# Kernel tuning notes

Measured on AMD Instinct MI355X. Metric: run time of the kernel, lower is better.

The kernel has to match this reference:

```python
import jax, jax.numpy as jnp
import numpy as np

N = 50000      # nodes
E = 600000     # edges
F_IN = 128     # input features
H = 128        # hidden
C = 40         # classes


def _glorot(key, shape):
    lim = float(np.sqrt(6.0 / (shape[0] + shape[1])))
    return jax.random.uniform(key, shape, jnp.float32, -lim, lim)


def setup_inputs() -> dict:
    key = jax.random.key(0)
    ks = jax.random.split(key, 16)
    inp = {
        "x": jax.random.normal(ks[0], (N, F_IN), jnp.float32),
        "edge_index": jax.random.randint(ks[1], (2, E), 0, N, jnp.int64),
    }
    # SAGEConv params: Wl (neighbor branch, with bias), Wr (root branch), stored [in, out]
    dims = [(F_IN, H), (H, H), (H, H)]
    for i, (din, dout) in enumerate(dims, start=1):
        inp[f"Wl{i}"] = _glorot(ks[2 * i], (din, dout))
        inp[f"bl{i}"] = jnp.zeros((dout,), jnp.float32)
        inp[f"Wr{i}"] = _glorot(ks[2 * i + 1], (din, dout))
    inp["W_lin1"] = _glorot(ks[10], (H, H))
    inp["b_lin1"] = jnp.zeros((H,), jnp.float32)
    inp["W_lin2"] = _glorot(ks[11], (H, C))
    inp["b_lin2"] = jnp.zeros((C,), jnp.float32)
    return inp


def _sage_conv(x, src, dst, Wl, bl, Wr):
    # mean-aggregate neighbor features at destination nodes
    msgs = x[src]  # [E, d] gather
    agg = jax.ops.segment_sum(msgs, dst, num_segments=N)
    deg = jax.ops.segment_sum(jnp.ones((E,), x.dtype), dst, num_segments=N)
    agg = agg / jnp.clip(deg, 1.0)[:, None]
    return agg @ Wl + bl + x @ Wr


def reference(x, edge_index, Wl1, bl1, Wr1, Wl2, bl2, Wr2, Wl3, bl3, Wr3,
              W_lin1, b_lin1, W_lin2, b_lin2):
    src, dst = edge_index[0], edge_index[1]
    h = jax.nn.relu(_sage_conv(x, src, dst, Wl1, bl1, Wr1))
    h = jax.nn.relu(_sage_conv(h, src, dst, Wl2, bl2, Wr2))
    h = jax.nn.relu(_sage_conv(h, src, dst, Wl3, bl3, Wr3))
    h = jax.nn.relu(h @ W_lin1 + b_lin1)
    # dropout: inference mode (training=False) -> identity
    logits = h @ W_lin2 + b_lin2
    return jax.nn.log_softmax(logits, axis=-1)
```

## Files before the change

### kernel.cpp

```cpp
#include <hip/hip_runtime.h>
#include <hip/hip_bf16.h>
#include <math.h>

#define NNODES 50000
#define NEDGES 600000
#define FDIM   128
#define NCLS   40
#define SLOTS  64
#define FILL_BLOCKS 1172
#define CVT_BLOCKS 6250
#define PACK_BLOCKS 62
#define ALL_TOTAL (FILL_BLOCKS + CVT_BLOCKS + PACK_BLOCKS)
#define NT16 (NNODES / 16)

typedef __hip_bfloat16 bf16;
typedef short bf16x8 __attribute__((ext_vector_type(8)));
typedef short bf16x4 __attribute__((ext_vector_type(4)));
typedef float f32x4  __attribute__((ext_vector_type(4)));
typedef float f32x2  __attribute__((ext_vector_type(2)));
typedef unsigned u32x4 __attribute__((ext_vector_type(4)));

__device__ __forceinline__ float u2f(unsigned u) {
    union { unsigned i; float f; } cv;
    cv.i = u;
    return cv.f;
}
__device__ __forceinline__ short f2b(float f) {
    bf16 h = __float2bfloat16(f);
    return *(const short*)&h;
}
__device__ __forceinline__ float ldf(const void* p, int fp32, int idx) {
    return fp32 ? ((const float*)p)[idx]
                : __bfloat162float(((const bf16*)p)[idx]);
}
__device__ __forceinline__ int wave_is_fp32(const unsigned* p, int lane) {
    unsigned w = p[lane];
    unsigned e = (w >> 7) & 0xFFu;
    int inr = (e >= 100u && e <= 140u) ? 1 : 0;
    return (int)__popcll(__ballot(inr)) < 32;
}
__device__ __forceinline__ int lidx(int row, int col) {
    return row * 128 + ((((col >> 3) ^ (row & 15)) << 3) | (col & 7));
}

__global__ void k_all(const int* __restrict__ e32, const long long* __restrict__ e64,
                      const void* __restrict__ xin,
                      const void* Wl1, const void* Wr1, const void* Wl2,
                      const void* Wr2, const void* Wl3, const void* Wr3,
                      const void* Wlin1, const void* Wlin2,
                      const void* b1, const void* b2, const void* b3,
                      const void* b4, const void* b5,
                      int* __restrict__ cursor, int* __restrict__ edge_src,
                      bf16* __restrict__ xb,
                      bf16x8* __restrict__ packed, float* __restrict__ biasf) {
    int b = blockIdx.x, tid = threadIdx.x, lane = tid & 63;
    if (b < FILL_BLOCKS) {
        unsigned hw = ((const unsigned*)e32)[2 * lane + 1];
        int is64 = (__ballot(hw != 0u) == 0ull) ? 1 : 0;
        int i0 = b * 512 + tid;
        int i1 = i0 + 256;
        int s0 = 0, d0 = 0, s1 = 0, d1 = 0;
        bool v0 = i0 < NEDGES, v1 = i1 < NEDGES;
        if (v0) { s0 = is64 ? (int)e64[i0] : e32[i0];
                  d0 = is64 ? (int)e64[NEDGES + i0] : e32[NEDGES + i0]; }
        if (v1) { s1 = is64 ? (int)e64[i1] : e32[i1];
                  d1 = is64 ? (int)e64[NEDGES + i1] : e32[NEDGES + i1]; }
        int p0 = 0, p1 = 0;
        if (v0) p0 = atomicAdd(&cursor[d0], 1);
        if (v1) p1 = atomicAdd(&cursor[d1], 1);
        if (v0 && p0 < SLOTS) edge_src[d0 * SLOTS + p0] = s0;
        if (v1 && p1 < SLOTS) edge_src[d1 * SLOTS + p1] = s1;
        return;
    }
    if (b < FILL_BLOCKS + CVT_BLOCKS) {
        int xf = wave_is_fp32((const unsigned*)xin, lane);
        int i = (b - FILL_BLOCKS) * 256 + tid;
        if (xf) {
            float4 v = ((const float4*)xin)[i];
            bf16x4 o;
            o[0] = f2b(v.x); o[1] = f2b(v.y); o[2] = f2b(v.z); o[3] = f2b(v.w);
            ((bf16x4*)xb)[i] = o;
        } else {
            ((uint2*)xb)[i] = ((const uint2*)xin)[i];
        }
        return;
    }
    int wf = wave_is_fp32((const unsigned*)Wl1, lane);
    int lb = b - FILL_BLOCKS - CVT_BLOCKS;
    if (lb >= 59) {
        int t = (lb - 59) * 256 + tid;
        if (t >= 5 * 128) return;
        int which = t >> 7, idx = t & 127;
        const void* srcs[5] = {b1, b2, b3, b4, b5};
        int n = (which == 4) ? NCLS : 128;
        float v = 0.f;
        if (idx < n) v = ldf(srcs[which], wf, idx);
        biasf[t] = v;
        return;
    }
    int t2 = lb * 256 + tid;
    int frag = t2 >> 6;
    if (frag >= 236) return;
    int q = lane >> 4, l16 = lane & 15;
    const void* W;
    int kbase, n, ldw = 128, nvalid = 128;
    if (frag < 192) {
        int g = frag >> 6, local = frag & 63;
        int kt = local >> 3, nt = local & 7;
        const void* Wl = (g == 0) ? Wl1 : (g == 1) ? Wl2 : Wl3;
        const void* Wr = (g == 0) ? Wr1 : (g == 1) ? Wr2 : Wr3;
        W = (kt < 4) ? Wl : Wr;
        kbase = (kt & 3) * 32;
        n = nt * 16 + l16;
    } else if (frag < 224) {
        int local = frag - 192;
        int kt = local >> 3, nt = local & 7;
        W = Wlin1; kbase = kt * 32; n = nt * 16 + l16;
    } else {
        int local = frag - 224;
        int kt = local / 3, nt = local % 3;
        W = Wlin2; kbase = kt * 32; n = nt * 16 + l16;
        ldw = NCLS; nvalid = NCLS;
    }
    bf16x8 v;
#pragma unroll
    for (int j = 0; j < 8; j++) {
        float e = 0.f;
        if (n < nvalid) e = ldf(W, wf, (kbase + q * 8 + j) * ldw + n);
        v[j] = f2b(e);
    }
    packed[frag * 64 + lane] = v;
}

__device__ __forceinline__ void agg8(const bf16* __restrict__ x,
        const int* __restrict__ deg, const int* __restrict__ es,
        short* __restrict__ lds, int node00, int wave, int lane) {
    const int g = lane >> 4, c = lane & 15;
    const int gsel = lane & 48;
    const int nbase = node00 + wave * 8;
    int dgp[2], eip[2];
#pragma unroll
    for (int p = 0; p < 2; p++) dgp[p] = deg[nbase + p * 4 + g];
#pragma unroll
    for (int p = 0; p < 2; p++) {
        int ei = es[(nbase + p * 4 + g) * SLOTS + c];
        eip[p] = ((unsigned)ei >= NNODES) ? 0 : ei;
    }
#pragma unroll
    for (int p = 0; p < 2; p++) {
        const int dg = dgp[p];
        f32x2 acc2[4];
#pragma unroll
        for (int k = 0; k < 4; k++) acc2[k] = (f32x2){0.f, 0.f};
#pragma unroll
        for (int j = 0; j < 16; j++) {
            int idx = __shfl(eip[p], gsel | j);
            float m = (j < dg) ? 1.f : 0.f;
            f32x2 m2 = (f32x2){m, m};
            u32x4 u = *(const u32x4*)(x + (unsigned)(idx * FDIM + c * 8));
#pragma unroll
            for (int k = 0; k < 4; k++) {
                f32x2 vv = (f32x2){u2f(u[k] << 16), u2f(u[k] & 0xFFFF0000u)};
                acc2[k] += vv * m2;
            }
        }
        if (__ballot(dg > 16) != 0ull) {
            for (int jb = 16; jb < SLOTS && __ballot(dg > jb) != 0ull; jb += 16) {
                int ei2 = es[(nbase + p * 4 + g) * SLOTS + jb + c];
                if ((unsigned)ei2 >= NNODES) ei2 = 0;
                for (int j = 0; j < 16; j++) {
                    int idx = __shfl(ei2, gsel | j);
                    float m = (jb + j < dg) ? 1.f : 0.f;
                    f32x2 m2 = (f32x2){m, m};
                    u32x4 u = *(const u32x4*)(x + (unsigned)(idx * FDIM + c * 8));
#pragma unroll
                    for (int k = 0; k < 4; k++) {
                        f32x2 vv = (f32x2){u2f(u[k] << 16), u2f(u[k] & 0xFFFF0000u)};
                        acc2[k] += vv * m2;
                    }
                }
            }
        }
        float inv = (dg > 0) ? 1.f / (float)dg : 0.f;
        bf16x8 o;
#pragma unroll
        for (int k = 0; k < 4; k++) {
            o[2 * k]     = f2b(acc2[k].x * inv);
            o[2 * k + 1] = f2b(acc2[k].y * inv);
        }
        *(bf16x8*)(lds + lidx(wave * 8 + p * 4 + g, c * 8)) = o;
    }
}

__device__ __forceinline__ void gemm_half(int lane, int wave,
        short* __restrict__ lds, const bf16x8 rt[4],
        const bf16x8* __restrict__ packed, const float* __restrict__ bias) {
    const int q = lane >> 4, l16 = lane & 15;
    f32x4 acc[4];
#pragma unroll
    for (int n = 0; n < 4; n++) acc[n] = (f32x4){0.f, 0.f, 0.f, 0.f};
#pragma unroll
    for (int kt = 0; kt < 8; kt++) {
        bf16x8 a;
        if (kt < 4)
            a = *(const bf16x8*)(lds + lidx(l16, kt * 32 + q * 8));
        else
            a = rt[kt - 4];
#pragma unroll
        for (int n = 0; n < 4; n++)
            acc[n] = __builtin_amdgcn_mfma_f32_16x16x32_bf16(
                a, packed[(kt * 8 + wave * 4 + n) * 64 + lane], acc[n], 0, 0, 0);
    }
    __syncthreads();
#pragma unroll
    for (int n = 0; n < 4; n++) {
        int col = (wave * 4 + n) * 16 + l16;
        float bv = bias[col];
#pragma unroll
        for (int r = 0; r < 4; r++)
            lds[lidx(q * 4 + r, col)] = f2b(fmaxf(acc[n][r] + bv, 0.f));
    }
    __syncthreads();
}

__device__ __forceinline__ void store_half(int rowbase, int lane, int wave,
        const short* __restrict__ lds, bf16* __restrict__ out) {
    const int g = lane >> 4, c = lane & 15;
#pragma unroll
    for (int pp = 0; pp < 2; pp++) {
        int p = wave * 2 + pp;
        bf16x8 v = *(const bf16x8*)(lds + lidx(p * 4 + g, c * 8));
        *(bf16x8*)(out + (unsigned)((rowbase + p * 4 + g) * FDIM + c * 8)) = v;
    }
}

__device__ __forceinline__ void head(int rowbase, int lane, int wave,
        const short* __restrict__ h3, short* __restrict__ h1,
        const bf16x8* __restrict__ packed, const float* __restrict__ bias1,
        const float* __restrict__ bias2, float* __restrict__ out) {
    const int q = lane >> 4, l16 = lane & 15;
    f32x4 acc[4];
#pragma unroll
    for (int n = 0; n < 4; n++) acc[n] = (f32x4){0.f, 0.f, 0.f, 0.f};
#pragma unroll
    for (int kt = 0; kt < 4; kt++) {
        bf16x8 a = *(const bf16x8*)(h3 + lidx(l16, kt * 32 + q * 8));
#pragma unroll
        for (int n = 0; n < 4; n++)
            acc[n] = __builtin_amdgcn_mfma_f32_16x16x32_bf16(
                a, packed[(192 + kt * 8 + wave * 4 + n) * 64 + lane], acc[n], 0, 0, 0);
    }
#pragma unroll
    for (int n = 0; n < 4; n++) {
        int col = (wave * 4 + n) * 16 + l16;
        float bv = bias1[col];
#pragma unroll
        for (int r = 0; r < 4; r++)
            h1[lidx(q * 4 + r, col)] = f2b(fmaxf(acc[n][r] + bv, 0.f));
    }
    __syncthreads();
    if (wave != 0) return;
    f32x4 acc2[3];
#pragma unroll
    for (int n = 0; n < 3; n++) acc2[n] = (f32x4){0.f, 0.f, 0.f, 0.f};
#pragma unroll
    for (int kt = 0; kt < 4; kt++) {
        bf16x8 a = *(const bf16x8*)(h1 + lidx(l16, kt * 32 + q * 8));
#pragma unroll
        for (int n = 0; n < 3; n++)
            acc2[n] = __builtin_amdgcn_mfma_f32_16x16x32_bf16(
                a, packed[(224 + kt * 3 + n) * 64 + lane], acc2[n], 0, 0, 0);
    }
    const float NEG = -1e30f;
    bool v2ok = (l16 < 8);
#pragma unroll
    for (int r = 0; r < 4; r++) {
        unsigned row = (unsigned)(rowbase + q * 4 + r);
        float v0 = acc2[0][r] + bias2[l16];
        float v1 = acc2[1][r] + bias2[16 + l16];
        float v2 = v2ok ? (acc2[2][r] + bias2[32 + l16]) : NEG;
        float m = fmaxf(fmaxf(v0, v1), v2);
#pragma unroll
        for (int mk = 1; mk < 16; mk <<= 1) m = fmaxf(m, __shfl_xor(m, mk));
        float sden = expf(v0 - m) + expf(v1 - m) + (v2ok ? expf(v2 - m) : 0.f);
#pragma unroll
        for (int mk = 1; mk < 16; mk <<= 1) sden += __shfl_xor(sden, mk);
        float l = m + logf(sden);
        out[row * NCLS + l16] = v0 - l;
        out[row * NCLS + 16 + l16] = v1 - l;
        if (v2ok) out[row * NCLS + 32 + l16] = v2 - l;
    }
}

__global__ void __launch_bounds__(128)
k_layer(const bf16* __restrict__ src, const int* __restrict__ deg,
        const int* __restrict__ edge_src, const bf16x8* __restrict__ packed,
        const float* __restrict__ bias, bf16* __restrict__ out) {
    __shared__ __align__(16) short lds[16 * 128];
    const int lane = threadIdx.x & 63, wave = threadIdx.x >> 6;
    const int rowbase = blockIdx.x * 16;
    const int q = lane >> 4, l16 = lane & 15;
    bf16x8 rt[4];
#pragma unroll
    for (int kt = 0; kt < 4; kt++)
        rt[kt] = *(const bf16x8*)(src +
                     (unsigned)((rowbase + l16) * FDIM + kt * 32 + q * 8));
    agg8(src, deg, edge_src, lds, rowbase, wave, lane);
    __syncthreads();
    gemm_half(lane, wave, lds, rt, packed, bias);
    store_half(rowbase, lane, wave, lds, out);
}

__global__ void __launch_bounds__(128)
k_layer3head(const bf16* __restrict__ src, const int* __restrict__ deg,
             const int* __restrict__ edge_src, const bf16x8* __restrict__ packed,
             const float* __restrict__ biasf, float* __restrict__ out) {
    __shared__ __align__(16) short h3[16 * 128];
    __shared__ __align__(16) short h1[16 * 128];
    const int lane = threadIdx.x & 63, wave = threadIdx.x >> 6;
    const int rowbase = blockIdx.x * 16;
    const int q = lane >> 4, l16 = lane & 15;
    bf16x8 rt[4];
#pragma unroll
    for (int kt = 0; kt < 4; kt++)
        rt[kt] = *(const bf16x8*)(src +
                     (unsigned)((rowbase + l16) * FDIM + kt * 32 + q * 8));
    agg8(src, deg, edge_src, h3, rowbase, wave, lane);
    __syncthreads();
    gemm_half(lane, wave, h3, rt, packed + 128 * 64, biasf + 256);
    head(rowbase, lane, wave, h3, h1, packed, biasf + 384, biasf + 512, out);
}

extern "C" void kernel_launch(void* const* d_in, const int* in_sizes, int n_in,
                              void* d_out, int out_size, void* d_ws, size_t ws_size,
                              hipStream_t stream) {
    char* ws = (char*)d_ws;
    size_t off = 0;
    auto take = [&](size_t bytes) {
        void* pp = ws + off;
        off = (off + bytes + 255) & ~(size_t)255;
        return pp;
    };
    const int* e32 = (const int*)d_in[1];
    const long long* e64 = (const long long*)d_in[1];
    int* cursor    = (int*)take(NNODES * 4);
    int* edge_src  = (int*)take((size_t)NNODES * SLOTS * 4);
    bf16x8* packed = (bf16x8*)take(236 * 64 * 16);
    float* biasf   = (float*)take(5 * 128 * 4);
    bf16* xb       = (bf16*)take((size_t)NNODES * FDIM * 2);
    bf16* bufA     = (bf16*)take((size_t)NNODES * FDIM * 2);
    float* outp    = (float*)d_out;
    bf16* bufB     = xb;

    hipMemsetAsync(cursor, 0, NNODES * 4, stream);
    k_all<<<ALL_TOTAL, 256, 0, stream>>>(
        e32, e64, d_in[0], d_in[2], d_in[4], d_in[5], d_in[7], d_in[8],
        d_in[10], d_in[11], d_in[13], d_in[3], d_in[6], d_in[9], d_in[12],
        d_in[14], cursor, edge_src, xb, packed, biasf);

    k_layer<<<NT16, 128, 0, stream>>>(xb, cursor, edge_src, packed, biasf, bufA);
    k_layer<<<NT16, 128, 0, stream>>>(bufA, cursor, edge_src,
                                      packed + 64 * 64, biasf + 128, bufB);
    k_layer3head<<<NT16, 128, 0, stream>>>(bufB, cursor, edge_src,
                                           packed, biasf, outp);
}
```

Measured before the change: 230.0 us.

## Precompute layer-1 root GEMM in prep kernel and use 4-wave layer blocks

```diff
diff --git a/kernel.cpp b/kernel.cpp
--- a/kernel.cpp
+++ b/kernel.cpp
@@ -9,8 +9,10 @@
 #define SLOTS  64
 #define FILL_BLOCKS 1172
 #define CVT_BLOCKS 6250
-#define PACK_BLOCKS 62
-#define ALL_TOTAL (FILL_BLOCKS + CVT_BLOCKS + PACK_BLOCKS)
+#define R1_BLOCKS 3125
+#define ALL_TOTAL (FILL_BLOCKS + CVT_BLOCKS + R1_BLOCKS)
+#define CZ_BLOCKS 49
+#define PRE_TOTAL (CZ_BLOCKS + 62)
 #define NT16 (NNODES / 16)
 
 typedef __hip_bfloat16 bf16;
@@ -43,50 +45,21 @@
     return row * 128 + ((((col >> 3) ^ (row & 15)) << 3) | (col & 7));
 }
 
-__global__ void k_all(const int* __restrict__ e32, const long long* __restrict__ e64,
-                      const void* __restrict__ xin,
-                      const void* Wl1, const void* Wr1, const void* Wl2,
+__global__ void k_pre(const void* Wl1, const void* Wr1, const void* Wl2,
                       const void* Wr2, const void* Wl3, const void* Wr3,
                       const void* Wlin1, const void* Wlin2,
                       const void* b1, const void* b2, const void* b3,
                       const void* b4, const void* b5,
-                      int* __restrict__ cursor, int* __restrict__ edge_src,
-                      bf16* __restrict__ xb,
+                      int* __restrict__ cursor,
                       bf16x8* __restrict__ packed, float* __restrict__ biasf) {
     int b = blockIdx.x, tid = threadIdx.x, lane = tid & 63;
-    if (b < FILL_BLOCKS) {
-        unsigned hw = ((const unsigned*)e32)[2 * lane + 1];
-        int is64 = (__ballot(hw != 0u) == 0ull) ? 1 : 0;
-        int i0 = b * 512 + tid;
-        int i1 = i0 + 256;
-        int s0 = 0, d0 = 0, s1 = 0, d1 = 0;
-        bool v0 = i0 < NEDGES, v1 = i1 < NEDGES;
-        if (v0) { s0 = is64 ? (int)e64[i0] : e32[i0];
-                  d0 = is64 ? (int)e64[NEDGES + i0] : e32[NEDGES + i0]; }
-        if (v1) { s1 = is64 ? (int)e64[i1] : e32[i1];
-                  d1 = is64 ? (int)e64[NEDGES + i1] : e32[NEDGES + i1]; }
-        int p0 = 0, p1 = 0;
-        if (v0) p0 = atomicAdd(&cursor[d0], 1);
-        if (v1) p1 = atomicAdd(&cursor[d1], 1);
-        if (v0 && p0 < SLOTS) edge_src[d0 * SLOTS + p0] = s0;
-        if (v1 && p1 < SLOTS) edge_src[d1 * SLOTS + p1] = s1;
+    if (b < CZ_BLOCKS) {
+        int i = b * 256 + tid;
+        if (i < NNODES / 4 + 1) ((int4*)cursor)[i] = (int4){0, 0, 0, 0};
         return;
     }
-    if (b < FILL_BLOCKS + CVT_BLOCKS) {
-        int xf = wave_is_fp32((const unsigned*)xin, lane);
-        int i = (b - FILL_BLOCKS) * 256 + tid;
-        if (xf) {
-            float4 v = ((const float4*)xin)[i];
-            bf16x4 o;
-            o[0] = f2b(v.x); o[1] = f2b(v.y); o[2] = f2b(v.z); o[3] = f2b(v.w);
-            ((bf16x4*)xb)[i] = o;
-        } else {
-            ((uint2*)xb)[i] = ((const uint2*)xin)[i];
-        }
-        return;
-    }
     int wf = wave_is_fp32((const unsigned*)Wl1, lane);
-    int lb = b - FILL_BLOCKS - CVT_BLOCKS;
+    int lb = b - CZ_BLOCKS;
     if (lb >= 59) {
         int t = (lb - 59) * 256 + tid;
         if (t >= 5 * 128) return;
@@ -132,106 +105,179 @@
     packed[frag * 64 + lane] = v;
 }
 
-__device__ __forceinline__ void agg8(const bf16* __restrict__ x,
+__global__ void k_all(const int* __restrict__ e32, const long long* __restrict__ e64,
+                      const void* __restrict__ xin,
+                      int* __restrict__ cursor, int* __restrict__ edge_src,
+                      bf16* __restrict__ xb,
+                      const bf16x8* __restrict__ packed,
+                      const float* __restrict__ biasf, float* __restrict__ R1) {
+    int b = blockIdx.x, tid = threadIdx.x, lane = tid & 63;
+    if (b < FILL_BLOCKS) {
+        unsigned hw = ((const unsigned*)e32)[2 * lane + 1];
+        int is64 = (__ballot(hw != 0u) == 0ull) ? 1 : 0;
+        int i0 = b * 512 + tid;
+        int i1 = i0 + 256;
+        int s0 = 0, d0 = 0, s1 = 0, d1 = 0;
+        bool v0 = i0 < NEDGES, v1 = i1 < NEDGES;
+        if (v0) { s0 = is64 ? (int)e64[i0] : e32[i0];
+                  d0 = is64 ? (int)e64[NEDGES + i0] : e32[NEDGES + i0]; }
+        if (v1) { s1 = is64 ? (int)e64[i1] : e32[i1];
+                  d1 = is64 ? (int)e64[NEDGES + i1] : e32[NEDGES + i1]; }
+        int p0 = 0, p1 = 0;
+        if (v0) p0 = atomicAdd(&cursor[d0], 1);
+        if (v1) p1 = atomicAdd(&cursor[d1], 1);
+        if (v0 && p0 < SLOTS) edge_src[d0 * SLOTS + p0] = s0;
+        if (v1 && p1 < SLOTS) edge_src[d1 * SLOTS + p1] = s1;
+        return;
+    }
+    if (b < FILL_BLOCKS + CVT_BLOCKS) {
+        int xf = wave_is_fp32((const unsigned*)xin, lane);
+        int i = (b - FILL_BLOCKS) * 256 + tid;
+        if (xf) {
+            float4 v = ((const float4*)xin)[i];
+            bf16x4 o;
+            o[0] = f2b(v.x); o[1] = f2b(v.y); o[2] = f2b(v.z); o[3] = f2b(v.w);
+            ((bf16x4*)xb)[i] = o;
+        } else {
+            ((uint2*)xb)[i] = ((const uint2*)xin)[i];
+        }
+        return;
+    }
+    int rb = (b - FILL_BLOCKS - CVT_BLOCKS) * 16;
+    int wave = tid >> 6;
+    int q = lane >> 4, l16 = lane & 15;
+    int xf = wave_is_fp32((const unsigned*)xin, lane);
+    bf16x8 a[4];
+#pragma unroll
+    for (int kt = 0; kt < 4; kt++) {
+        if (xf) {
+            const float* xp = (const float*)xin +
+                              (unsigned)((rb + l16) * FDIM + kt * 32 + q * 8);
+            float4 v0 = *(const float4*)xp;
+            float4 v1 = *(const float4*)(xp + 4);
+            a[kt][0] = f2b(v0.x); a[kt][1] = f2b(v0.y);
+            a[kt][2] = f2b(v0.z); a[kt][3] = f2b(v0.w);
+            a[kt][4] = f2b(v1.x); a[kt][5] = f2b(v1.y);
+            a[kt][6] = f2b(v1.z); a[kt][7] = f2b(v1.w);
+        } else {
+            a[kt] = *(const bf16x8*)((const bf16*)xin +
+                        (unsigned)((rb + l16) * FDIM + kt * 32 + q * 8));
+        }
+    }
+    f32x4 acc[2];
+#pragma unroll
+    for (int n = 0; n < 2; n++) acc[n] = (f32x4){0.f, 0.f, 0.f, 0.f};
+#pragma unroll
+    for (int kt = 0; kt < 4; kt++)
+#pragma unroll
+        for (int n = 0; n < 2; n++)
+            acc[n] = __builtin_amdgcn_mfma_f32_16x16x32_bf16(
+                a[kt], packed[((kt + 4) * 8 + wave * 2 + n) * 64 + lane],
+                acc[n], 0, 0, 0);
+#pragma unroll
+    for (int n = 0; n < 2; n++) {
+        int col = (wave * 2 + n) * 16 + l16;
+        float bv = biasf[col];
+#pragma unroll
+        for (int r = 0; r < 4; r++)
+            R1[(unsigned)((rb + q * 4 + r) * FDIM + col)] = acc[n][r] + bv;
+    }
+}
+
+__device__ __forceinline__ void agg4(const bf16* __restrict__ x,
         const int* __restrict__ deg, const int* __restrict__ es,
-        short* __restrict__ lds, int node00, int wave, int lane) {
+        short* __restrict__ lds, int rowbase, int wave, int lane) {
     const int g = lane >> 4, c = lane & 15;
     const int gsel = lane & 48;
-    const int nbase = node00 + wave * 8;
-    int dgp[2], eip[2];
-#pragma unroll
-    for (int p = 0; p < 2; p++) dgp[p] = deg[nbase + p * 4 + g];
-#pragma unroll
-    for (int p = 0; p < 2; p++) {
-        int ei = es[(nbase + p * 4 + g) * SLOTS + c];
-        eip[p] = ((unsigned)ei >= NNODES) ? 0 : ei;
-    }
-#pragma unroll
-    for (int p = 0; p < 2; p++) {
-        const int dg = dgp[p];
-        f32x2 acc2[4];
-#pragma unroll
-        for (int k = 0; k < 4; k++) acc2[k] = (f32x2){0.f, 0.f};
-#pragma unroll
-        for (int j = 0; j < 16; j++) {
-            int idx = __shfl(eip[p], gsel | j);
-            float m = (j < dg) ? 1.f : 0.f;
-            f32x2 m2 = (f32x2){m, m};
-            u32x4 u = *(const u32x4*)(x + (unsigned)(idx * FDIM + c * 8));
-#pragma unroll
-            for (int k = 0; k < 4; k++) {
-                f32x2 vv = (f32x2){u2f(u[k] << 16), u2f(u[k] & 0xFFFF0000u)};
-                acc2[k] += vv * m2;
-            }
+    const int node = rowbase + wave * 4 + g;
+    const int dg = deg[node];
+    int ei = es[node * SLOTS + c];
+    if ((unsigned)ei >= NNODES) ei = 0;
+    f32x2 acc2[4];
+#pragma unroll
+    for (int k = 0; k < 4; k++) acc2[k] = (f32x2){0.f, 0.f};
+#pragma unroll
+    for (int j = 0; j < 16; j++) {
+        int idx = __shfl(ei, gsel | j);
+        float m = (j < dg) ? 1.f : 0.f;
+        f32x2 m2 = (f32x2){m, m};
+        u32x4 u = *(const u32x4*)(x + (unsigned)(idx * FDIM + c * 8));
+#pragma unroll
+        for (int k = 0; k < 4; k++) {
+            f32x2 vv = (f32x2){u2f(u[k] << 16), u2f(u[k] & 0xFFFF0000u)};
+            acc2[k] += vv * m2;
         }
-        if (__ballot(dg > 16) != 0ull) {
-            for (int jb = 16; jb < SLOTS && __ballot(dg > jb) != 0ull; jb += 16) {
-                int ei2 = es[(nbase + p * 4 + g) * SLOTS + jb + c];
-                if ((unsigned)ei2 >= NNODES) ei2 = 0;
-                for (int j = 0; j < 16; j++) {
-                    int idx = __shfl(ei2, gsel | j);
-                    float m = (jb + j < dg) ? 1.f : 0.f;
-                    f32x2 m2 = (f32x2){m, m};
-                    u32x4 u = *(const u32x4*)(x + (unsigned)(idx * FDIM + c * 8));
-#pragma unroll
-                    for (int k = 0; k < 4; k++) {
-                        f32x2 vv = (f32x2){u2f(u[k] << 16), u2f(u[k] & 0xFFFF0000u)};
-                        acc2[k] += vv * m2;
-                    }
+    }
+    if (__ballot(dg > 16) != 0ull) {
+        for (int jb = 16; jb < SLOTS && __ballot(dg > jb) != 0ull; jb += 16) {
+            int ei2 = es[node * SLOTS + jb + c];
+            if ((unsigned)ei2 >= NNODES) ei2 = 0;
+            for (int j = 0; j < 16; j++) {
+                int idx = __shfl(ei2, gsel | j);
+                float m = (jb + j < dg) ? 1.f : 0.f;
+                f32x2 m2 = (f32x2){m, m};
+                u32x4 u = *(const u32x4*)(x + (unsigned)(idx * FDIM + c * 8));
+#pragma unroll
+                for (int k = 0; k < 4; k++) {
+                    f32x2 vv = (f32x2){u2f(u[k] << 16), u2f(u[k] & 0xFFFF0000u)};
+                    acc2[k] += vv * m2;
                 }
             }
         }
-        float inv = (dg > 0) ? 1.f / (float)dg : 0.f;
-        bf16x8 o;
-#pragma unroll
-        for (int k = 0; k < 4; k++) {
-            o[2 * k]     = f2b(acc2[k].x * inv);
-            o[2 * k + 1] = f2b(acc2[k].y * inv);
-        }
-        *(bf16x8*)(lds + lidx(wave * 8 + p * 4 + g, c * 8)) = o;
-    }
-}
-
-__device__ __forceinline__ void gemm_half(int lane, int wave,
+    }
+    float inv = (dg > 0) ? 1.f / (float)dg : 0.f;
+    bf16x8 o;
+#pragma unroll
+    for (int k = 0; k < 4; k++) {
+        o[2 * k]     = f2b(acc2[k].x * inv);
+        o[2 * k + 1] = f2b(acc2[k].y * inv);
+    }
+    *(bf16x8*)(lds + lidx(wave * 4 + g, c * 8)) = o;
+}
+
+template <bool FIRST>
+__device__ __forceinline__ void gemm_q(int rowbase, int lane, int wave,
         short* __restrict__ lds, const bf16x8 rt[4],
-        const bf16x8* __restrict__ packed, const float* __restrict__ bias) {
+        const bf16x8* __restrict__ packed, const float* __restrict__ bias,
+        const float* __restrict__ R1) {
     const int q = lane >> 4, l16 = lane & 15;
-    f32x4 acc[4];
-#pragma unroll
-    for (int n = 0; n < 4; n++) acc[n] = (f32x4){0.f, 0.f, 0.f, 0.f};
-#pragma unroll
-    for (int kt = 0; kt < 8; kt++) {
+    f32x4 acc[2];
+#pragma unroll
+    for (int n = 0; n < 2; n++) acc[n] = (f32x4){0.f, 0.f, 0.f, 0.f};
+    const int KT = FIRST ? 4 : 8;
+#pragma unroll
+    for (int kt = 0; kt < KT; kt++) {
         bf16x8 a;
         if (kt < 4)
             a = *(const bf16x8*)(lds + lidx(l16, kt * 32 + q * 8));
         else
             a = rt[kt - 4];
 #pragma unroll
-        for (int n = 0; n < 4; n++)
+        for (int n = 0; n < 2; n++)
             acc[n] = __builtin_amdgcn_mfma_f32_16x16x32_bf16(
-                a, packed[(kt * 8 + wave * 4 + n) * 64 + lane], acc[n], 0, 0, 0);
+                a, packed[(kt * 8 + wave * 2 + n) * 64 + lane], acc[n], 0, 0, 0);
     }
     __syncthreads();
 #pragma unroll
-    for (int n = 0; n < 4; n++) {
-        int col = (wave * 4 + n) * 16 + l16;
-        float bv = bias[col];
-#pragma unroll
-        for (int r = 0; r < 4; r++)
-            lds[lidx(q * 4 + r, col)] = f2b(fmaxf(acc[n][r] + bv, 0.f));
+    for (int n = 0; n < 2; n++) {
+        int col = (wave * 2 + n) * 16 + l16;
+        float bv = FIRST ? 0.f : bias[col];
+#pragma unroll
+        for (int r = 0; r < 4; r++) {
+            float v = acc[n][r] + bv;
+            if (FIRST) v += R1[(unsigned)((rowbase + q * 4 + r) * FDIM + col)];
+            lds[lidx(q * 4 + r, col)] = f2b(fmaxf(v, 0.f));
+        }
     }
     __syncthreads();
 }
 
-__device__ __forceinline__ void store_half(int rowbase, int lane, int wave,
+__device__ __forceinline__ void store_q(int rowbase, int lane, int wave,
         const short* __restrict__ lds, bf16* __restrict__ out) {
     const int g = lane >> 4, c = lane & 15;
-#pragma unroll
-    for (int pp = 0; pp < 2; pp++) {
-        int p = wave * 2 + pp;
-        bf16x8 v = *(const bf16x8*)(lds + lidx(p * 4 + g, c * 8));
-        *(bf16x8*)(out + (unsigned)((rowbase + p * 4 + g) * FDIM + c * 8)) = v;
-    }
+    int p = wave * 4 + g;
+    bf16x8 v = *(const bf16x8*)(lds + lidx(p, c * 8));
+    *(bf16x8*)(out + (unsigned)((rowbase + p) * FDIM + c * 8)) = v;
 }
 
 __device__ __forceinline__ void head(int rowbase, int lane, int wave,
@@ -239,20 +285,20 @@
         const bf16x8* __restrict__ packed, const float* __restrict__ bias1,
         const float* __restrict__ bias2, float* __restrict__ out) {
     const int q = lane >> 4, l16 = lane & 15;
-    f32x4 acc[4];
-#pragma unroll
-    for (int n = 0; n < 4; n++) acc[n] = (f32x4){0.f, 0.f, 0.f, 0.f};
+    f32x4 acc[2];
+#pragma unroll
+    for (int n = 0; n < 2; n++) acc[n] = (f32x4){0.f, 0.f, 0.f, 0.f};
 #pragma unroll
     for (int kt = 0; kt < 4; kt++) {
         bf16x8 a = *(const bf16x8*)(h3 + lidx(l16, kt * 32 + q * 8));
 #pragma unroll
-        for (int n = 0; n < 4; n++)
+        for (int n = 0; n < 2; n++)
             acc[n] = __builtin_amdgcn_mfma_f32_16x16x32_bf16(
-                a, packed[(192 + kt * 8 + wave * 4 + n) * 64 + lane], acc[n], 0, 0, 0);
-    }
-#pragma unroll
-    for (int n = 0; n < 4; n++) {
-        int col = (wave * 4 + n) * 16 + l16;
+                a, packed[(192 + kt * 8 + wave * 2 + n) * 64 + lane], acc[n], 0, 0, 0);
+    }
+#pragma unroll
+    for (int n = 0; n < 2; n++) {
+        int col = (wave * 2 + n) * 16 + l16;
         float bv = bias1[col];
 #pragma unroll
         for (int r = 0; r < 4; r++)
@@ -292,26 +338,30 @@
     }
 }
 
-__global__ void __launch_bounds__(128)
-k_layer(const bf16* __restrict__ src, const int* __restrict__ deg,
-        const int* __restrict__ edge_src, const bf16x8* __restrict__ packed,
-        const float* __restrict__ bias, bf16* __restrict__ out) {
+template <bool FIRST>
+__global__ void __launch_bounds__(256)
+k_layer_t(const bf16* __restrict__ src, const int* __restrict__ deg,
+          const int* __restrict__ edge_src, const bf16x8* __restrict__ packed,
+          const float* __restrict__ bias, const float* __restrict__ R1,
+          bf16* __restrict__ out) {
     __shared__ __align__(16) short lds[16 * 128];
     const int lane = threadIdx.x & 63, wave = threadIdx.x >> 6;
     const int rowbase = blockIdx.x * 16;
     const int q = lane >> 4, l16 = lane & 15;
     bf16x8 rt[4];
-#pragma unroll
-    for (int kt = 0; kt < 4; kt++)
-        rt[kt] = *(const bf16x8*)(src +
-                     (unsigned)((rowbase + l16) * FDIM + kt * 32 + q * 8));
-    agg8(src, deg, edge_src, lds, rowbase, wave, lane);
+    if (!FIRST) {
+#pragma unroll
+        for (int kt = 0; kt < 4; kt++)
+            rt[kt] = *(const bf16x8*)(src +
+                         (unsigned)((rowbase + l16) * FDIM + kt * 32 + q * 8));
+    }
+    agg4(src, deg, edge_src, lds, rowbase, wave, lane);
     __syncthreads();
-    gemm_half(lane, wave, lds, rt, packed, bias);
-    store_half(rowbase, lane, wave, lds, out);
-}
-
-__global__ void __launch_bounds__(128)
+    gemm_q<FIRST>(rowbase, lane, wave, lds, rt, packed, bias, R1);
+    store_q(rowbase, lane, wave, lds, out);
+}
+
+__global__ void __launch_bounds__(256)
 k_layer3head(const bf16* __restrict__ src, const int* __restrict__ deg,
              const int* __restrict__ edge_src, const bf16x8* __restrict__ packed,
              const float* __restrict__ biasf, float* __restrict__ out) {
@@ -325,9 +375,10 @@
     for (int kt = 0; kt < 4; kt++)
         rt[kt] = *(const bf16x8*)(src +
                      (unsigned)((rowbase + l16) * FDIM + kt * 32 + q * 8));
-    agg8(src, deg, edge_src, h3, rowbase, wave, lane);
+    agg4(src, deg, edge_src, h3, rowbase, wave, lane);
     __syncthreads();
-    gemm_half(lane, wave, h3, rt, packed + 128 * 64, biasf + 256);
+    gemm_q<false>(rowbase, lane, wave, h3, rt, packed + 128 * 64,
+                  biasf + 256, nullptr);
     head(rowbase, lane, wave, h3, h1, packed, biasf + 384, biasf + 512, out);
 }
 
@@ -343,24 +394,28 @@
     };
     const int* e32 = (const int*)d_in[1];
     const long long* e64 = (const long long*)d_in[1];
-    int* cursor    = (int*)take(NNODES * 4);
+    int* cursor    = (int*)take((NNODES + 16) * 4);
     int* edge_src  = (int*)take((size_t)NNODES * SLOTS * 4);
     bf16x8* packed = (bf16x8*)take(236 * 64 * 16);
     float* biasf   = (float*)take(5 * 128 * 4);
+    float* R1      = (float*)take((size_t)NNODES * FDIM * 4);
     bf16* xb       = (bf16*)take((size_t)NNODES * FDIM * 2);
     bf16* bufA     = (bf16*)take((size_t)NNODES * FDIM * 2);
     float* outp    = (float*)d_out;
     bf16* bufB     = xb;
 
-    hipMemsetAsync(cursor, 0, NNODES * 4, stream);
+    k_pre<<<PRE_TOTAL, 256, 0, stream>>>(
+        d_in[2], d_in[4], d_in[5], d_in[7], d_in[8], d_in[10], d_in[11],
+        d_in[13], d_in[3], d_in[6], d_in[9], d_in[12], d_in[14],
+        cursor, packed, biasf);
     k_all<<<ALL_TOTAL, 256, 0, stream>>>(
-        e32, e64, d_in[0], d_in[2], d_in[4], d_in[5], d_in[7], d_in[8],
-        d_in[10], d_in[11], d_in[13], d_in[3], d_in[6], d_in[9], d_in[12],
-        d_in[14], cursor, edge_src, xb, packed, biasf);
-
-    k_layer<<<NT16, 128, 0, stream>>>(xb, cursor, edge_src, packed, biasf, bufA);
-    k_layer<<<NT16, 128, 0, stream>>>(bufA, cursor, edge_src,
-                                      packed + 64 * 64, biasf + 128, bufB);
-    k_layer3head<<<NT16, 128, 0, stream>>>(bufB, cursor, edge_src,
+        e32, e64, d_in[0], cursor, edge_src, xb, packed, biasf, R1);
+
+    k_layer_t<true><<<NT16, 256, 0, stream>>>(xb, cursor, edge_src, packed,
+                                              biasf, R1, bufA);
+    k_layer_t<false><<<NT16, 256, 0, stream>>>(bufA, cursor, edge_src,
+                                               packed + 64 * 64, biasf + 128,
+                                               nullptr, bufB);
+    k_layer3head<<<NT16, 256, 0, stream>>>(bufB, cursor, edge_src,
                                            packed, biasf, outp);
 }
```

Result: slower. 243.7 us (+6.0%).
